# Kernel tuning notes

Measured on AMD Instinct MI355X. Metric: run time of the kernel, lower is better.

Reference implementation:

```python
import jax, jax.numpy as jnp
import numpy as np

D_MODEL, D_STATE, D_CONV, EXPAND = 1024, 16, 4, 2
D_INNER = D_MODEL * EXPAND
BATCH, SEQ_LEN = 2, 2048
LN_EPS = 1e-5


def setup_inputs() -> dict:
    key = jax.random.key(0)
    ks = jax.random.split(key, 10)
    s = lambda fan_in: 1.0 / np.sqrt(fan_in)
    x = jax.random.normal(ks[0], (BATCH, D_MODEL, SEQ_LEN), jnp.float32)
    ln_w = jnp.ones((D_MODEL,), jnp.float32)
    ln_b = jnp.zeros((D_MODEL,), jnp.float32)
    # Linear weights stored as [in, out]
    W_in = jax.random.normal(ks[1], (D_MODEL, 2 * D_INNER), jnp.float32) * s(D_MODEL)
    conv_w = jax.random.normal(ks[2], (D_INNER, 1, D_CONV), jnp.float32) * s(D_CONV)
    conv_b = jax.random.normal(ks[3], (D_INNER,), jnp.float32) * s(D_CONV)
    W_x = jax.random.normal(ks[4], (D_INNER, 2 * D_STATE + D_INNER), jnp.float32) * s(D_INNER)
    W_dt = jax.random.normal(ks[5], (D_INNER, D_INNER), jnp.float32) * s(D_INNER)
    b_dt = jax.random.normal(ks[6], (D_INNER,), jnp.float32) * s(D_INNER)
    A_log = jnp.broadcast_to(jnp.log(jnp.arange(1, D_STATE + 1, dtype=jnp.float32))[None, :], (D_INNER, D_STATE))
    Dskip = jnp.ones((D_INNER,), jnp.float32)
    W_out = jax.random.normal(ks[7], (D_INNER, D_MODEL), jnp.float32) * s(D_INNER)
    return {"x": x, "ln_w": ln_w, "ln_b": ln_b, "W_in": W_in, "conv_w": conv_w,
            "conv_b": conv_b, "W_x": W_x, "W_dt": W_dt, "b_dt": b_dt,
            "A_log": A_log, "Dskip": Dskip, "W_out": W_out}


def _selective_scan(u, delta, A, Bp, Cp, Dskip):
    # u, delta: [B, d_inner, L]; A: [d_inner, d_state]; Bp, Cp: [B, d_state, L]
    u_T = jnp.transpose(u, (2, 0, 1))        # [L, B, d_inner]
    d_T = jnp.transpose(delta, (2, 0, 1))    # [L, B, d_inner]
    B_T = jnp.transpose(Bp, (2, 0, 1))       # [L, B, d_state]
    C_T = jnp.transpose(Cp, (2, 0, 1))       # [L, B, d_state]
    h0 = jnp.zeros((u.shape[0], u.shape[1], A.shape[1]), u.dtype)

    def step(h, inp):
        dlt_t, B_t, C_t, u_t = inp
        dA = jnp.exp(dlt_t[..., None] * A)                       # [B, d_inner, d_state]
        h = dA * h + dlt_t[..., None] * B_t[:, None, :] * u_t[..., None]
        y_t = jnp.einsum('bds,bs->bd', h, C_t)
        return h, y_t

    _, ys = jax.lax.scan(step, h0, (d_T, B_T, C_T, u_T))
    y = jnp.transpose(ys, (1, 2, 0))  # [B, d_inner, L]
    return y + Dskip[None, :, None] * u


def reference(x, ln_w, ln_b, W_in, conv_w, conv_b, W_x, W_dt, b_dt, A_log, Dskip, W_out):
    residual = x
    xt = jnp.swapaxes(x, 1, 2)  # [B, L, d_model]
    mu = xt.mean(-1, keepdims=True)
    var = ((xt - mu) ** 2).mean(-1, keepdims=True)
    xn = (xt - mu) * jax.lax.rsqrt(var + LN_EPS) * ln_w + ln_b
    xz = xn @ W_in                                   # [B, L, 2*d_inner]
    xb, z = jnp.split(xz, 2, axis=-1)
    xb = jnp.swapaxes(xb, 1, 2)                      # [B, d_inner, L]
    # causal depthwise conv (torch pads d_conv-1 both sides then slices [:L])
    xb = jax.lax.conv_general_dilated(
        xb, conv_w, window_strides=(1,), padding=[(D_CONV - 1, 0)],
        dimension_numbers=('NCH', 'OIH', 'NCH'), feature_group_count=D_INNER)
    xb = xb + conv_b[None, :, None]
    xb = jax.nn.silu(xb)
    xbt = jnp.swapaxes(xb, 1, 2)                     # [B, L, d_inner]
    bcd = xbt @ W_x                                  # [B, L, 2*d_state + d_inner]
    Bp = bcd[..., :D_STATE]
    Cp = bcd[..., D_STATE:2 * D_STATE]
    dlt = jax.nn.softplus(bcd[..., 2 * D_STATE:] @ W_dt + b_dt)
    Bp = jnp.swapaxes(Bp, 1, 2)                      # [B, d_state, L]
    Cp = jnp.swapaxes(Cp, 1, 2)
    dlt = jnp.swapaxes(dlt, 1, 2)                    # [B, d_inner, L]
    A = -jnp.exp(A_log)
    y = _selective_scan(xb, dlt, A, Bp, Cp, Dskip)   # [B, d_inner, L]
    y = jnp.swapaxes(y, 1, 2) * jax.nn.silu(z)       # [B, L, d_inner]
    out = y @ W_out                                  # [B, L, d_model]
    return jnp.swapaxes(out, 1, 2) + residual
```

## Files before the change

### kernel.cpp

```cpp
#include <hip/hip_runtime.h>
#include <cstdint>
#include <cstddef>

#define SEQL 2048
#define DMODEL 1024
#define DINNER 2048
#define NSTATE 16
#define NC 32
#define TC 64
#define KS 16
#define KCH 128

typedef __attribute__((ext_vector_type(4))) float f32x4;
typedef __attribute__((ext_vector_type(8))) short short8;
typedef __attribute__((ext_vector_type(4))) short short4v;
typedef unsigned short u16;

__device__ __forceinline__ float b2f(u16 u) {
  union { unsigned int i; float f; } v; v.i = ((unsigned int)u) << 16; return v.f;
}
__device__ __forceinline__ u16 f2b(float f) {
  union { float f; unsigned int i; } v; v.f = f;
  unsigned int r = v.i + 0x7FFFu + ((v.i >> 16) & 1u);
  return (u16)(r >> 16);
}

__global__ __launch_bounds__(256) void k_transpose_cvt(
    const float* __restrict__ in, u16* __restrict__ out, int R, int C, int c0) {
  __shared__ float t[32][33];
  int cb = blockIdx.x * 32, rb = blockIdx.y * 32;
  int tx = threadIdx.x, ty = threadIdx.y;
#pragma unroll
  for (int i = 0; i < 32; i += 8)
    t[ty + i][tx] = in[(size_t)(rb + ty + i) * C + c0 + cb + tx];
  __syncthreads();
#pragma unroll
  for (int i = 0; i < 32; i += 8)
    out[(size_t)(cb + ty + i) * R + rb + tx] = f2b(t[tx][ty + i]);
}

__global__ __launch_bounds__(256) void k_layernorm(
    const u16* __restrict__ xt, const float* __restrict__ w,
    const float* __restrict__ b, u16* __restrict__ xn) {
  int row = blockIdx.x;
  const u16* px = xt + (size_t)row * DMODEL;
  int i4 = threadIdx.x * 4;
  short4v sv = *(const short4v*)&px[i4];
  float v[4];
#pragma unroll
  for (int j = 0; j < 4; ++j) v[j] = b2f((u16)sv[j]);
  float s1 = v[0] + v[1] + v[2] + v[3];
  float s2 = v[0]*v[0] + v[1]*v[1] + v[2]*v[2] + v[3]*v[3];
#pragma unroll
  for (int off = 32; off > 0; off >>= 1) {
    s1 += __shfl_xor(s1, off);
    s2 += __shfl_xor(s2, off);
  }
  __shared__ float a1[4], a2[4];
  int lane = threadIdx.x & 63, wid = threadIdx.x >> 6;
  if (lane == 0) { a1[wid] = s1; a2[wid] = s2; }
  __syncthreads();
  float t1 = a1[0] + a1[1] + a1[2] + a1[3];
  float t2 = a2[0] + a2[1] + a2[2] + a2[3];
  float mu = t1 * (1.f / DMODEL);
  float rs = rsqrtf(t2 * (1.f / DMODEL) - mu * mu + 1e-5f);
  short4v ov;
#pragma unroll
  for (int j = 0; j < 4; ++j) ov[j] = (short)f2b((v[j] - mu) * rs * w[i4 + j] + b[i4 + j]);
  *(short4v*)&xn[(size_t)row * DMODEL + i4] = ov;
}

template<int EPI>
__global__ __launch_bounds__(256) void gemm8p(
    const u16* __restrict__ A, const u16* __restrict__ BT,
    void* __restrict__ outp, const float* __restrict__ bias,
    const float* __restrict__ resid, int M, int N, int K) {
  constexpr int LDSTILE = 2 * 128 * 64;
  __shared__ u16 lds[2 * LDSTILE];

  const int tid = threadIdx.x;
  const int w = tid >> 6, lane = tid & 63;
  const int wm = w >> 1, wn = w & 1;
  const int lg = lane >> 4, lr = lane & 15;
  const int wbase = tid & ~63;

  const int gx = N / 128;
  const int cpx = gridDim.x >> 3;
  const int wg = ((int)blockIdx.x & 7) * cpx + ((int)blockIdx.x >> 3);
  const int tm = (wg / gx) * 128;
  const int tn = (wg % gx) * 128;
  const int NT = K >> 6;

  const u16* Ab = A + (size_t)tm * K;
  const u16* Bb = BT + (size_t)tn * K;

  auto stage = [&](const u16* gbase, int boff, int tc, int h) {
    int tcl = tc < NT ? tc : NT - 1;
    const u16* g0 = gbase + (size_t)tcl * 64;
    u16* l0 = lds + (tc & 1) * LDSTILE + boff;
#pragma unroll
    for (int j = 0; j < 2; ++j) {
      int t8 = j * 256 + tid;
      int r8 = t8 >> 3;
      int pr = (r8 & 31) + ((r8 >> 5) << 6) + h * 32;
      int sk = ((((t8 & 7) << 4) ^ ((pr & 7) << 4)) >> 1);
      int r8b = (j * 256 + wbase) >> 3;
      int prb = (r8b & 31) + ((r8b >> 5) << 6) + h * 32;
      __builtin_amdgcn_global_load_lds(
          (const __attribute__((address_space(1))) void*)(g0 + (size_t)pr * K + sk),
          (__attribute__((address_space(3))) void*)(l0 + prb * 64), 16, 0, 0);
    }
  };
  auto fragA = [&](int buf, int mf, int kk) -> short8 {
    int r = wm * 64 + mf * 16 + lr;
    int cb = (kk * 64 + lg * 16) ^ ((r & 7) << 4);
    return *(const short8*)((const char*)(lds + buf * LDSTILE) + r * 128 + cb);
  };
  auto fragB = [&](int buf, int nf, int kk) -> short8 {
    int r = wn * 64 + nf * 16 + lr;
    int cb = (kk * 64 + lg * 16) ^ ((r & 7) << 4);
    return *(const short8*)((const char*)(lds + buf * LDSTILE + 128 * 64) + r * 128 + cb);
  };

  f32x4 acc[4][4] = {};
  short8 aF[2][2], bF0[2][2], bF1[2][2];

  stage(Ab, 0, 0, 0); stage(Bb, 128 * 64, 0, 0);
  stage(Bb, 128 * 64, 0, 1); stage(Ab, 0, 0, 1);
  stage(Ab, 0, 1, 0); stage(Bb, 128 * 64, 1, 0);
  asm volatile("s_waitcnt vmcnt(4)" ::: "memory");
  __builtin_amdgcn_s_barrier();

  for (int t = 0; t < NT; ++t) {
    const int buf = t & 1;
#pragma unroll
    for (int mf = 0; mf < 2; ++mf) { aF[mf][0] = fragA(buf, mf, 0); aF[mf][1] = fragA(buf, mf, 1); }
#pragma unroll
    for (int nf = 0; nf < 2; ++nf) { bF0[nf][0] = fragB(buf, nf, 0); bF0[nf][1] = fragB(buf, nf, 1); }
    stage(Bb, 128 * 64, t + 1, 1);
    __builtin_amdgcn_s_barrier();
    asm volatile("s_waitcnt lgkmcnt(0)" ::: "memory");
    __builtin_amdgcn_s_setprio(1);
#pragma unroll
    for (int mf = 0; mf < 2; ++mf)
#pragma unroll
      for (int nf = 0; nf < 2; ++nf) {
        acc[mf][nf] = __builtin_amdgcn_mfma_f32_16x16x32_bf16(aF[mf][0], bF0[nf][0], acc[mf][nf], 0, 0, 0);
        acc[mf][nf] = __builtin_amdgcn_mfma_f32_16x16x32_bf16(aF[mf][1], bF0[nf][1], acc[mf][nf], 0, 0, 0);
      }
    __builtin_amdgcn_s_setprio(0);
    __builtin_amdgcn_s_barrier();
#pragma unroll
    for (int nf = 0; nf < 2; ++nf) { bF1[nf][0] = fragB(buf, 2 + nf, 0); bF1[nf][1] = fragB(buf, 2 + nf, 1); }
    stage(Ab, 0, t + 1, 1);
    __builtin_amdgcn_s_barrier();
    asm volatile("s_waitcnt lgkmcnt(0)" ::: "memory");
    __builtin_amdgcn_s_setprio(1);
#pragma unroll
    for (int mf = 0; mf < 2; ++mf)
#pragma unroll
      for (int nf = 0; nf < 2; ++nf) {
        acc[mf][2 + nf] = __builtin_amdgcn_mfma_f32_16x16x32_bf16(aF[mf][0], bF1[nf][0], acc[mf][2 + nf], 0, 0, 0);
        acc[mf][2 + nf] = __builtin_amdgcn_mfma_f32_16x16x32_bf16(aF[mf][1], bF1[nf][1], acc[mf][2 + nf], 0, 0, 0);
      }
    __builtin_amdgcn_s_setprio(0);
    __builtin_amdgcn_s_barrier();
#pragma unroll
    for (int mf = 0; mf < 2; ++mf) { aF[mf][0] = fragA(buf, 2 + mf, 0); aF[mf][1] = fragA(buf, 2 + mf, 1); }
    stage(Ab, 0, t + 2, 0);
    __builtin_amdgcn_s_barrier();
    asm volatile("s_waitcnt lgkmcnt(0)" ::: "memory");
    __builtin_amdgcn_s_setprio(1);
#pragma unroll
    for (int mf = 0; mf < 2; ++mf)
#pragma unroll
      for (int nf = 0; nf < 2; ++nf) {
        acc[2 + mf][nf] = __builtin_amdgcn_mfma_f32_16x16x32_bf16(aF[mf][0], bF0[nf][0], acc[2 + mf][nf], 0, 0, 0);
        acc[2 + mf][nf] = __builtin_amdgcn_mfma_f32_16x16x32_bf16(aF[mf][1], bF0[nf][1], acc[2 + mf][nf], 0, 0, 0);
      }
    __builtin_amdgcn_s_setprio(0);
    __builtin_amdgcn_s_barrier();
    stage(Bb, 128 * 64, t + 2, 0);
    __builtin_amdgcn_s_barrier();
    asm volatile("s_waitcnt lgkmcnt(0)" ::: "memory");
    __builtin_amdgcn_s_setprio(1);
#pragma unroll
    for (int mf = 0; mf < 2; ++mf)
#pragma unroll
      for (int nf = 0; nf < 2; ++nf) {
        acc[2 + mf][2 + nf] = __builtin_amdgcn_mfma_f32_16x16x32_bf16(aF[mf][0], bF1[nf][0], acc[2 + mf][2 + nf], 0, 0, 0);
        acc[2 + mf][2 + nf] = __builtin_amdgcn_mfma_f32_16x16x32_bf16(aF[mf][1], bF1[nf][1], acc[2 + mf][2 + nf], 0, 0, 0);
      }
    __builtin_amdgcn_s_setprio(0);
    asm volatile("s_waitcnt vmcnt(4)" ::: "memory");
    __builtin_amdgcn_s_barrier();
  }

#pragma unroll
  for (int mf = 0; mf < 4; ++mf) {
    int r0 = tm + wm * 64 + mf * 16 + lg * 4;
#pragma unroll
    for (int nf = 0; nf < 4; ++nf) {
      int c = tn + wn * 64 + nf * 16 + lr;
      f32x4 v = acc[mf][nf];
#pragma unroll
      for (int j = 0; j < 4; ++j) {
        int r = r0 + j;
        if constexpr (EPI == 1) {
          ((u16*)outp)[(size_t)r * N + c] = f2b(v[j]);
        } else if constexpr (EPI == 2) {
          float xv = v[j] + bias[c];
          ((float*)outp)[(size_t)r * N + c] = (xv > 20.f) ? xv : log1pf(__expf(xv));
        } else if constexpr (EPI == 3) {
          int bb = r >> 11, tt = r & (SEQL - 1);
          size_t oi = ((size_t)(bb * N + c)) * SEQL + tt;
          ((float*)outp)[oi] = v[j] + resid[oi];
        } else {
          ((float*)outp)[(size_t)r * N + c] = v[j];
        }
      }
    }
  }
}

__global__ __launch_bounds__(256) void k_conv_silu(
    const u16* __restrict__ xz, const float* __restrict__ cw,
    const float* __restrict__ cb, u16* __restrict__ xbt) {
  size_t idx = (size_t)blockIdx.x * 256 + threadIdx.x;
  int d = (int)(idx & (DINNER - 1));
  int l = (int)((idx >> 11) & (SEQL - 1));
  int b = (int)(idx >> 22);
  f32x4 w = *(const f32x4*)&cw[d * 4];
  float acc = cb[d];
  size_t base = ((size_t)b * SEQL) * 4096 + d;
#pragma unroll
  for (int i = 0; i < 4; ++i) {
    int ls = l - 3 + i;
    if (ls >= 0) acc += w[i] * b2f(xz[base + (size_t)ls * 4096]);
  }
  float s = acc / (1.f + __expf(-acc));
  xbt[idx] = f2b(s);
}

__global__ __launch_bounds__(256) void k_bc_mfma(
    const u16* __restrict__ xbt, const u16* __restrict__ WxBCT,
    float* __restrict__ bcp) {
  __shared__ u16 As[128 * 32];
  int tid = threadIdx.x;
  int w = tid >> 6, lane = tid & 63;
  int tm = blockIdx.x * 128;
  int k0 = blockIdx.y * KCH;
  int lg = lane >> 4, lr = lane & 15;
  int srow = lane >> 2, scol = (lane & 3) * 8;

  f32x4 acc[2][2] = {};

  for (int kk = k0; kk < k0 + KCH; kk += 32) {
#pragma unroll
    for (int j = 0; j < 2; ++j) {
      int ch = w * 2 + j;
      const u16* ga = xbt + (size_t)(tm + ch * 16 + srow) * DINNER + kk + scol;
      __builtin_amdgcn_global_load_lds(
          (const __attribute__((address_space(1))) void*)ga,
          (__attribute__((address_space(3))) void*)&As[ch * 512], 16, 0, 0);
    }
    __syncthreads();
    short8 aF[2], bF[2];
#pragma unroll
    for (int m = 0; m < 2; ++m)
      aF[m] = *(const short8*)&As[(w * 32 + m * 16 + lr) * 32 + lg * 8];
#pragma unroll
    for (int n = 0; n < 2; ++n)
      bF[n] = *(const short8*)&WxBCT[(size_t)(n * 16 + lr) * DINNER + kk + lg * 8];
#pragma unroll
    for (int m = 0; m < 2; ++m)
#pragma unroll
      for (int n = 0; n < 2; ++n)
        acc[m][n] = __builtin_amdgcn_mfma_f32_16x16x32_bf16(aF[m], bF[n], acc[m][n], 0, 0, 0);
    __syncthreads();
  }

  float* outp = bcp + (size_t)blockIdx.y * (4096 * 32);
#pragma unroll
  for (int m = 0; m < 2; ++m) {
    int r0 = tm + w * 32 + m * 16 + lg * 4;
#pragma unroll
    for (int n = 0; n < 2; ++n) {
      int c = n * 16 + lr;
      f32x4 v = acc[m][n];
#pragma unroll
      for (int j = 0; j < 4; ++j)
        outp[(size_t)(r0 + j) * 32 + c] = v[j];
    }
  }
}

__global__ __launch_bounds__(256) void k_bc_red(
    const float* __restrict__ bcp, float* __restrict__ bc) {
  size_t i = (size_t)blockIdx.x * 256 + threadIdx.x;
  float s = 0.f;
#pragma unroll
  for (int ks = 0; ks < KS; ++ks)
    s += bcp[(size_t)ks * (4096 * 32) + i];
  bc[i] = s;
}

__global__ __launch_bounds__(256) void k_scan_p1(
    const float* __restrict__ dlt, const u16* __restrict__ ub,
    const float* __restrict__ bcv, const float* __restrict__ A_log,
    float* __restrict__ Pc, float* __restrict__ Qc) {
  int d = blockIdx.x * 256 + threadIdx.x;
  int c = blockIdx.y;
  int b = blockIdx.z;
  float Av[16];
#pragma unroll
  for (int sv = 0; sv < 4; ++sv) {
    f32x4 al = *(const f32x4*)&A_log[d * 16 + sv * 4];
#pragma unroll
    for (int j = 0; j < 4; ++j) Av[sv * 4 + j] = -__expf(al[j]);
  }
  float P[16], Q[16];
#pragma unroll
  for (int s = 0; s < 16; ++s) { P[s] = 1.f; Q[s] = 0.f; }
  size_t row0 = (size_t)b * SEQL + (size_t)c * TC;
  for (int t = 0; t < TC; ++t) {
    size_t row = row0 + t;
    float dl = dlt[row * DINNER + d];
    float uu = b2f(ub[row * DINNER + d]);
    float bco = dl * uu;
    const f32x4* Bp = (const f32x4*)&bcv[row * 32];
#pragma unroll
    for (int sv = 0; sv < 4; ++sv) {
      f32x4 Bv = Bp[sv];
#pragma unroll
      for (int j = 0; j < 4; ++j) {
        int s = sv * 4 + j;
        float dA = __expf(dl * Av[s]);
        P[s] *= dA;
        Q[s] = dA * Q[s] + bco * Bv[j];
      }
    }
  }
  size_t base = (((size_t)b * NC + c) * DINNER + d) * 16;
#pragma unroll
  for (int sv = 0; sv < 4; ++sv) {
    f32x4 pv, qv;
#pragma unroll
    for (int j = 0; j < 4; ++j) { pv[j] = P[sv * 4 + j]; qv[j] = Q[sv * 4 + j]; }
    *(f32x4*)&Pc[base + sv * 4] = pv;
    *(f32x4*)&Qc[base + sv * 4] = qv;
  }
}

__global__ __launch_bounds__(256) void k_scan_p2(
    const float* __restrict__ Pc, const float* __restrict__ Qc,
    float* __restrict__ Hs) {
  size_t gid = (size_t)blockIdx.x * 256 + threadIdx.x;
  size_t bds = gid & ((size_t)DINNER * 16 - 1);
  int b = (int)(gid >> 15);
  float h = 0.f;
  size_t cstride = (size_t)DINNER * 16;
  size_t base = (size_t)b * NC * cstride + bds;
  for (int c = 0; c < NC; ++c) {
    size_t idx = base + (size_t)c * cstride;
    Hs[idx] = h;
    h = Pc[idx] * h + Qc[idx];
  }
}

__global__ __launch_bounds__(256) void k_scan_p3(
    const float* __restrict__ dlt, const u16* __restrict__ ub,
    const float* __restrict__ bcv, const u16* __restrict__ xz,
    const float* __restrict__ A_log, const float* __restrict__ Dskip,
    const float* __restrict__ Hs, u16* __restrict__ yg) {
  int d = blockIdx.x * 256 + threadIdx.x;
  int c = blockIdx.y;
  int b = blockIdx.z;
  float Av[16];
#pragma unroll
  for (int sv = 0; sv < 4; ++sv) {
    f32x4 al = *(const f32x4*)&A_log[d * 16 + sv * 4];
#pragma unroll
    for (int j = 0; j < 4; ++j) Av[sv * 4 + j] = -__expf(al[j]);
  }
  float h[16];
  size_t hb = (((size_t)b * NC + c) * DINNER + d) * 16;
#pragma unroll
  for (int sv = 0; sv < 4; ++sv) {
    f32x4 hv = *(const f32x4*)&Hs[hb + sv * 4];
#pragma unroll
    for (int j = 0; j < 4; ++j) h[sv * 4 + j] = hv[j];
  }
  float Dsk = Dskip[d];
  size_t row0 = (size_t)b * SEQL + (size_t)c * TC;
  for (int t = 0; t < TC; ++t) {
    size_t row = row0 + t;
    float dl = dlt[row * DINNER + d];
    float uu = b2f(ub[row * DINNER + d]);
    float bco = dl * uu;
    const f32x4* BCp = (const f32x4*)&bcv[row * 32];
    float y = 0.f;
#pragma unroll
    for (int sv = 0; sv < 4; ++sv) {
      f32x4 Bv = BCp[sv];
      f32x4 Cv = BCp[4 + sv];
#pragma unroll
      for (int j = 0; j < 4; ++j) {
        int s = sv * 4 + j;
        float dA = __expf(dl * Av[s]);
        h[s] = dA * h[s] + bco * Bv[j];
        y += h[s] * Cv[j];
      }
    }
    float zv = b2f(xz[row * 4096 + DINNER + d]);
    float yv = (y + Dsk * uu) * (zv / (1.f + __expf(-zv)));
    yg[row * DINNER + d] = f2b(yv);
  }
}

extern "C" void kernel_launch(void* const* d_in, const int* in_sizes, int n_in,
                              void* d_out, int out_size, void* d_ws, size_t ws_size,
                              hipStream_t stream) {
  (void)in_sizes; (void)n_in; (void)out_size; (void)ws_size;
  const float* x      = (const float*)d_in[0];
  const float* ln_w   = (const float*)d_in[1];
  const float* ln_b   = (const float*)d_in[2];
  const float* W_in   = (const float*)d_in[3];
  const float* conv_w = (const float*)d_in[4];
  const float* conv_b = (const float*)d_in[5];
  const float* W_x    = (const float*)d_in[6];
  const float* W_dt   = (const float*)d_in[7];
  const float* b_dt   = (const float*)d_in[8];
  const float* A_log  = (const float*)d_in[9];
  const float* Dskip  = (const float*)d_in[10];
  const float* W_out  = (const float*)d_in[11];
  float* out = (float*)d_out;

  char* ws = (char*)d_ws;
  const size_t MB = 1048576;
  u16*  xt    = (u16*)(ws + 0 * MB);
  u16*  xn    = (u16*)(ws + 8 * MB);
  u16*  WinT  = (u16*)(ws + 16 * MB);
  u16*  WxT   = (u16*)(ws + 24 * MB);
  u16*  WdtT  = (u16*)(ws + 32 * MB);
  u16*  WoutT = (u16*)(ws + 40 * MB);
  u16*  xz    = (u16*)(ws + 44 * MB);
  u16*  xbt   = (u16*)(ws + 76 * MB);
  float* bc   = (float*)(ws + 92 * MB);
  u16*  dtin  = (u16*)(ws + 93 * MB);
  float* dlt  = (float*)(ws + 109 * MB);
  float* Pc   = (float*)(ws + 141 * MB);
  float* Qc   = (float*)(ws + 149 * MB);
  float* Hs   = (float*)(ws + 157 * MB);
  float* bcp  = (float*)(ws + 165 * MB);
  u16*  WxBCT = (u16*)(ws + 173 * MB);
  u16*  yg    = (u16*)(ws + 0 * MB);

  dim3 tb(32, 8);
  for (int b = 0; b < 2; ++b)
    k_transpose_cvt<<<dim3(SEQL / 32, DMODEL / 32), tb, 0, stream>>>(
        x + (size_t)b * DMODEL * SEQL, xt + (size_t)b * SEQL * DMODEL, DMODEL, SEQL, 0);
  k_transpose_cvt<<<dim3(4096 / 32, 1024 / 32), tb, 0, stream>>>(W_in, WinT, 1024, 4096, 0);
  k_transpose_cvt<<<dim3(2048 / 32, 2048 / 32), tb, 0, stream>>>(W_x, WxT, 2048, 2080, 32);
  k_transpose_cvt<<<dim3(1, 2048 / 32), tb, 0, stream>>>(W_x, WxBCT, 2048, 2080, 0);
  k_transpose_cvt<<<dim3(2048 / 32, 2048 / 32), tb, 0, stream>>>(W_dt, WdtT, 2048, 2048, 0);
  k_transpose_cvt<<<dim3(1024 / 32, 2048 / 32), tb, 0, stream>>>(W_out, WoutT, 2048, 1024, 0);

  k_layernorm<<<4096, 256, 0, stream>>>(xt, ln_w, ln_b, xn);

  gemm8p<1><<<1024, 256, 0, stream>>>(xn, WinT, xz, nullptr, nullptr, 4096, 4096, 1024);

  k_conv_silu<<<32768, 256, 0, stream>>>(xz, conv_w, conv_b, xbt);

  k_bc_mfma<<<dim3(4096 / 128, KS), 256, 0, stream>>>(xbt, WxBCT, bcp);
  k_bc_red<<<131072 / 256, 256, 0, stream>>>(bcp, bc);

  gemm8p<1><<<512, 256, 0, stream>>>(xbt, WxT, dtin, nullptr, nullptr, 4096, 2048, 2048);

  gemm8p<2><<<512, 256, 0, stream>>>(dtin, WdtT, dlt, b_dt, nullptr, 4096, 2048, 2048);

  k_scan_p1<<<dim3(DINNER / 256, NC, 2), 256, 0, stream>>>(dlt, xbt, bc, A_log, Pc, Qc);
  k_scan_p2<<<256, 256, 0, stream>>>(Pc, Qc, Hs);
  k_scan_p3<<<dim3(DINNER / 256, NC, 2), 256, 0, stream>>>(
      dlt, xbt, bc, xz, A_log, Dskip, Hs, yg);

  gemm8p<3><<<256, 256, 0, stream>>>(yg, WoutT, out, nullptr, x, 4096, 1024, 2048);
}
```

Baseline: 335.0 us.

## Fold W_x and W_dt into one weight, precompute GEMM addresses, vectorize conv

The delta path now multiplies the two weight matrices once (W_dt^T · W_x-slice^T) into a combined 2048x2048 matrix, replacing two activation GEMMs with one weight GEMM plus one activation GEMM. The GEMM kernel precomputes per-thread global and LDS addresses and unrolls the K loop by two so fixed buffer offsets replace per-iteration index math. The conv+silu kernel now handles two channels per thread with paired bf16 loads and stores. The weight product is computed in bf16 on every call, which adds rounding error on the delta path.

```diff
diff --git a/kernel.cpp b/kernel.cpp
--- a/kernel.cpp
+++ b/kernel.cpp
@@ -37,6 +37,18 @@
 #pragma unroll
   for (int i = 0; i < 32; i += 8)
     out[(size_t)(cb + ty + i) * R + rb + tx] = f2b(t[tx][ty + i]);
+}
+
+__global__ __launch_bounds__(256) void k_cvt_rows(
+    const float* __restrict__ in, u16* __restrict__ out) {
+  size_t idx = (size_t)blockIdx.x * 256 + threadIdx.x;
+  size_t i4 = idx * 4;
+  int r = (int)(i4 >> 11), c = (int)(i4 & 2047);
+  f32x4 v = *(const f32x4*)&in[(size_t)r * 2080 + 32 + c];
+  short4v o;
+#pragma unroll
+  for (int j = 0; j < 4; ++j) o[j] = (short)f2b(v[j]);
+  *(short4v*)&out[i4] = o;
 }
 
 __global__ __launch_bounds__(256) void k_layernorm(
@@ -91,109 +103,134 @@
   const int tn = (wg % gx) * 128;
   const int NT = K >> 6;
 
-  const u16* Ab = A + (size_t)tm * K;
-  const u16* Bb = BT + (size_t)tn * K;
-
-  auto stage = [&](const u16* gbase, int boff, int tc, int h) {
-    int tcl = tc < NT ? tc : NT - 1;
-    const u16* g0 = gbase + (size_t)tcl * 64;
-    u16* l0 = lds + (tc & 1) * LDSTILE + boff;
-#pragma unroll
-    for (int j = 0; j < 2; ++j) {
-      int t8 = j * 256 + tid;
-      int r8 = t8 >> 3;
-      int pr = (r8 & 31) + ((r8 >> 5) << 6) + h * 32;
-      int sk = ((((t8 & 7) << 4) ^ ((pr & 7) << 4)) >> 1);
-      int r8b = (j * 256 + wbase) >> 3;
-      int prb = (r8b & 31) + ((r8b >> 5) << 6) + h * 32;
+  const u16* aSp[2];
+  const u16* bSp[2];
+  int aD[2], bD[2];
+#pragma unroll
+  for (int j = 0; j < 2; ++j) {
+    int t8 = j * 256 + tid;
+    int r8 = t8 >> 3;
+    int pr = (r8 & 31) + ((r8 >> 5) << 6);
+    int sk = ((((t8 & 7) << 4) ^ ((pr & 7) << 4)) >> 1);
+    aSp[j] = A + (size_t)(tm + pr) * K + sk;
+    bSp[j] = BT + (size_t)(tn + pr) * K + sk;
+    int r8b = (j * 256 + wbase) >> 3;
+    int prb = (r8b & 31) + ((r8b >> 5) << 6);
+    aD[j] = prb * 64;
+    bD[j] = 128 * 64 + prb * 64;
+  }
+  int aFo[4][2], bFo[4][2];
+#pragma unroll
+  for (int mf = 0; mf < 4; ++mf)
+#pragma unroll
+    for (int kk = 0; kk < 2; ++kk) {
+      int r = wm * 64 + mf * 16 + lr;
+      aFo[mf][kk] = r * 128 + ((kk * 64 + lg * 16) ^ ((r & 7) << 4));
+      int rb = wn * 64 + mf * 16 + lr;
+      bFo[mf][kk] = 128 * 64 * 2 + rb * 128 + ((kk * 64 + lg * 16) ^ ((rb & 7) << 4));
+    }
+
+  auto stA = [&](int toff, int h, int buf) {
+#pragma unroll
+    for (int j = 0; j < 2; ++j)
       __builtin_amdgcn_global_load_lds(
-          (const __attribute__((address_space(1))) void*)(g0 + (size_t)pr * K + sk),
-          (__attribute__((address_space(3))) void*)(l0 + prb * 64), 16, 0, 0);
-    }
+          (const __attribute__((address_space(1))) void*)(aSp[j] + toff * 64 + h * (K << 5)),
+          (__attribute__((address_space(3))) void*)(lds + buf * LDSTILE + aD[j] + h * 2048),
+          16, 0, 0);
   };
-  auto fragA = [&](int buf, int mf, int kk) -> short8 {
-    int r = wm * 64 + mf * 16 + lr;
-    int cb = (kk * 64 + lg * 16) ^ ((r & 7) << 4);
-    return *(const short8*)((const char*)(lds + buf * LDSTILE) + r * 128 + cb);
-  };
-  auto fragB = [&](int buf, int nf, int kk) -> short8 {
-    int r = wn * 64 + nf * 16 + lr;
-    int cb = (kk * 64 + lg * 16) ^ ((r & 7) << 4);
-    return *(const short8*)((const char*)(lds + buf * LDSTILE + 128 * 64) + r * 128 + cb);
+  auto stB = [&](int toff, int h, int buf) {
+#pragma unroll
+    for (int j = 0; j < 2; ++j)
+      __builtin_amdgcn_global_load_lds(
+          (const __attribute__((address_space(1))) void*)(bSp[j] + toff * 64 + h * (K << 5)),
+          (__attribute__((address_space(3))) void*)(lds + buf * LDSTILE + bD[j] + h * 2048),
+          16, 0, 0);
   };
 
   f32x4 acc[4][4] = {};
   short8 aF[2][2], bF0[2][2], bF1[2][2];
 
-  stage(Ab, 0, 0, 0); stage(Bb, 128 * 64, 0, 0);
-  stage(Bb, 128 * 64, 0, 1); stage(Ab, 0, 0, 1);
-  stage(Ab, 0, 1, 0); stage(Bb, 128 * 64, 1, 0);
+  stA(0, 0, 0); stB(0, 0, 0); stB(0, 1, 0); stA(0, 1, 0);
+  stA(1, 0, 1); stB(1, 0, 1);
   asm volatile("s_waitcnt vmcnt(4)" ::: "memory");
   __builtin_amdgcn_s_barrier();
 
-  for (int t = 0; t < NT; ++t) {
-    const int buf = t & 1;
-#pragma unroll
-    for (int mf = 0; mf < 2; ++mf) { aF[mf][0] = fragA(buf, mf, 0); aF[mf][1] = fragA(buf, mf, 1); }
-#pragma unroll
-    for (int nf = 0; nf < 2; ++nf) { bF0[nf][0] = fragB(buf, nf, 0); bF0[nf][1] = fragB(buf, nf, 1); }
-    stage(Bb, 128 * 64, t + 1, 1);
-    __builtin_amdgcn_s_barrier();
-    asm volatile("s_waitcnt lgkmcnt(0)" ::: "memory");
-    __builtin_amdgcn_s_setprio(1);
-#pragma unroll
-    for (int mf = 0; mf < 2; ++mf)
-#pragma unroll
-      for (int nf = 0; nf < 2; ++nf) {
-        acc[mf][nf] = __builtin_amdgcn_mfma_f32_16x16x32_bf16(aF[mf][0], bF0[nf][0], acc[mf][nf], 0, 0, 0);
-        acc[mf][nf] = __builtin_amdgcn_mfma_f32_16x16x32_bf16(aF[mf][1], bF0[nf][1], acc[mf][nf], 0, 0, 0);
-      }
-    __builtin_amdgcn_s_setprio(0);
-    __builtin_amdgcn_s_barrier();
-#pragma unroll
-    for (int nf = 0; nf < 2; ++nf) { bF1[nf][0] = fragB(buf, 2 + nf, 0); bF1[nf][1] = fragB(buf, 2 + nf, 1); }
-    stage(Ab, 0, t + 1, 1);
-    __builtin_amdgcn_s_barrier();
-    asm volatile("s_waitcnt lgkmcnt(0)" ::: "memory");
-    __builtin_amdgcn_s_setprio(1);
-#pragma unroll
-    for (int mf = 0; mf < 2; ++mf)
-#pragma unroll
-      for (int nf = 0; nf < 2; ++nf) {
-        acc[mf][2 + nf] = __builtin_amdgcn_mfma_f32_16x16x32_bf16(aF[mf][0], bF1[nf][0], acc[mf][2 + nf], 0, 0, 0);
-        acc[mf][2 + nf] = __builtin_amdgcn_mfma_f32_16x16x32_bf16(aF[mf][1], bF1[nf][1], acc[mf][2 + nf], 0, 0, 0);
-      }
-    __builtin_amdgcn_s_setprio(0);
-    __builtin_amdgcn_s_barrier();
-#pragma unroll
-    for (int mf = 0; mf < 2; ++mf) { aF[mf][0] = fragA(buf, 2 + mf, 0); aF[mf][1] = fragA(buf, 2 + mf, 1); }
-    stage(Ab, 0, t + 2, 0);
-    __builtin_amdgcn_s_barrier();
-    asm volatile("s_waitcnt lgkmcnt(0)" ::: "memory");
-    __builtin_amdgcn_s_setprio(1);
-#pragma unroll
-    for (int mf = 0; mf < 2; ++mf)
-#pragma unroll
-      for (int nf = 0; nf < 2; ++nf) {
-        acc[2 + mf][nf] = __builtin_amdgcn_mfma_f32_16x16x32_bf16(aF[mf][0], bF0[nf][0], acc[2 + mf][nf], 0, 0, 0);
-        acc[2 + mf][nf] = __builtin_amdgcn_mfma_f32_16x16x32_bf16(aF[mf][1], bF0[nf][1], acc[2 + mf][nf], 0, 0, 0);
-      }
-    __builtin_amdgcn_s_setprio(0);
-    __builtin_amdgcn_s_barrier();
-    stage(Bb, 128 * 64, t + 2, 0);
-    __builtin_amdgcn_s_barrier();
-    asm volatile("s_waitcnt lgkmcnt(0)" ::: "memory");
-    __builtin_amdgcn_s_setprio(1);
-#pragma unroll
-    for (int mf = 0; mf < 2; ++mf)
-#pragma unroll
-      for (int nf = 0; nf < 2; ++nf) {
-        acc[2 + mf][2 + nf] = __builtin_amdgcn_mfma_f32_16x16x32_bf16(aF[mf][0], bF1[nf][0], acc[2 + mf][2 + nf], 0, 0, 0);
-        acc[2 + mf][2 + nf] = __builtin_amdgcn_mfma_f32_16x16x32_bf16(aF[mf][1], bF1[nf][1], acc[2 + mf][2 + nf], 0, 0, 0);
-      }
-    __builtin_amdgcn_s_setprio(0);
-    asm volatile("s_waitcnt vmcnt(4)" ::: "memory");
-    __builtin_amdgcn_s_barrier();
+  for (int tt = 0; tt < NT; tt += 2) {
+#pragma unroll
+    for (int u = 0; u < 2; ++u) {
+      const char* Lb = (const char*)lds + u * (LDSTILE * 2);
+#pragma unroll
+      for (int mf = 0; mf < 2; ++mf)
+#pragma unroll
+        for (int kk = 0; kk < 2; ++kk) aF[mf][kk] = *(const short8*)(Lb + aFo[mf][kk]);
+#pragma unroll
+      for (int nf = 0; nf < 2; ++nf)
+#pragma unroll
+        for (int kk = 0; kk < 2; ++kk) bF0[nf][kk] = *(const short8*)(Lb + bFo[nf][kk]);
+      stB(u + 1, 1, (u + 1) & 1);
+      __builtin_amdgcn_s_barrier();
+      asm volatile("s_waitcnt lgkmcnt(0)" ::: "memory");
+      __builtin_amdgcn_s_setprio(1);
+#pragma unroll
+      for (int mf = 0; mf < 2; ++mf)
+#pragma unroll
+        for (int nf = 0; nf < 2; ++nf) {
+          acc[mf][nf] = __builtin_amdgcn_mfma_f32_16x16x32_bf16(aF[mf][0], bF0[nf][0], acc[mf][nf], 0, 0, 0);
+          acc[mf][nf] = __builtin_amdgcn_mfma_f32_16x16x32_bf16(aF[mf][1], bF0[nf][1], acc[mf][nf], 0, 0, 0);
+        }
+      __builtin_amdgcn_s_setprio(0);
+      __builtin_amdgcn_s_barrier();
+#pragma unroll
+      for (int nf = 0; nf < 2; ++nf)
+#pragma unroll
+        for (int kk = 0; kk < 2; ++kk) bF1[nf][kk] = *(const short8*)(Lb + bFo[2 + nf][kk]);
+      stA(u + 1, 1, (u + 1) & 1);
+      __builtin_amdgcn_s_barrier();
+      asm volatile("s_waitcnt lgkmcnt(0)" ::: "memory");
+      __builtin_amdgcn_s_setprio(1);
+#pragma unroll
+      for (int mf = 0; mf < 2; ++mf)
+#pragma unroll
+        for (int nf = 0; nf < 2; ++nf) {
+          acc[mf][2 + nf] = __builtin_amdgcn_mfma_f32_16x16x32_bf16(aF[mf][0], bF1[nf][0], acc[mf][2 + nf], 0, 0, 0);
+          acc[mf][2 + nf] = __builtin_amdgcn_mfma_f32_16x16x32_bf16(aF[mf][1], bF1[nf][1], acc[mf][2 + nf], 0, 0, 0);
+        }
+      __builtin_amdgcn_s_setprio(0);
+      __builtin_amdgcn_s_barrier();
+#pragma unroll
+      for (int mf = 0; mf < 2; ++mf)
+#pragma unroll
+        for (int kk = 0; kk < 2; ++kk) aF[mf][kk] = *(const short8*)(Lb + aFo[2 + mf][kk]);
+      stA(u + 2, 0, u & 1);
+      __builtin_amdgcn_s_barrier();
+      asm volatile("s_waitcnt lgkmcnt(0)" ::: "memory");
+      __builtin_amdgcn_s_setprio(1);
+#pragma unroll
+      for (int mf = 0; mf < 2; ++mf)
+#pragma unroll
+        for (int nf = 0; nf < 2; ++nf) {
+          acc[2 + mf][nf] = __builtin_amdgcn_mfma_f32_16x16x32_bf16(aF[mf][0], bF0[nf][0], acc[2 + mf][nf], 0, 0, 0);
+          acc[2 + mf][nf] = __builtin_amdgcn_mfma_f32_16x16x32_bf16(aF[mf][1], bF0[nf][1], acc[2 + mf][nf], 0, 0, 0);
+        }
+      __builtin_amdgcn_s_setprio(0);
+      __builtin_amdgcn_s_barrier();
+      stB(u + 2, 0, u & 1);
+      __builtin_amdgcn_s_barrier();
+      asm volatile("s_waitcnt lgkmcnt(0)" ::: "memory");
+      __builtin_amdgcn_s_setprio(1);
+#pragma unroll
+      for (int mf = 0; mf < 2; ++mf)
+#pragma unroll
+        for (int nf = 0; nf < 2; ++nf) {
+          acc[2 + mf][2 + nf] = __builtin_amdgcn_mfma_f32_16x16x32_bf16(aF[mf][0], bF1[nf][0], acc[2 + mf][2 + nf], 0, 0, 0);
+          acc[2 + mf][2 + nf] = __builtin_amdgcn_mfma_f32_16x16x32_bf16(aF[mf][1], bF1[nf][1], acc[2 + mf][2 + nf], 0, 0, 0);
+        }
+      __builtin_amdgcn_s_setprio(0);
+      asm volatile("s_waitcnt vmcnt(4)" ::: "memory");
+      __builtin_amdgcn_s_barrier();
+    }
+#pragma unroll
+    for (int j = 0; j < 2; ++j) { aSp[j] += 128; bSp[j] += 128; }
   }
 
 #pragma unroll
@@ -212,8 +249,8 @@
           float xv = v[j] + bias[c];
           ((float*)outp)[(size_t)r * N + c] = (xv > 20.f) ? xv : log1pf(__expf(xv));
         } else if constexpr (EPI == 3) {
-          int bb = r >> 11, tt = r & (SEQL - 1);
-          size_t oi = ((size_t)(bb * N + c)) * SEQL + tt;
+          int bb = r >> 11, tt2 = r & (SEQL - 1);
+          size_t oi = ((size_t)(bb * N + c)) * SEQL + tt2;
           ((float*)outp)[oi] = v[j] + resid[oi];
         } else {
           ((float*)outp)[(size_t)r * N + c] = v[j];
@@ -227,19 +264,27 @@
     const u16* __restrict__ xz, const float* __restrict__ cw,
     const float* __restrict__ cb, u16* __restrict__ xbt) {
   size_t idx = (size_t)blockIdx.x * 256 + threadIdx.x;
-  int d = (int)(idx & (DINNER - 1));
-  int l = (int)((idx >> 11) & (SEQL - 1));
-  int b = (int)(idx >> 22);
-  f32x4 w = *(const f32x4*)&cw[d * 4];
-  float acc = cb[d];
-  size_t base = ((size_t)b * SEQL) * 4096 + d;
+  int d2 = (int)(idx & (DINNER / 2 - 1));
+  int d = d2 * 2;
+  int l = (int)((idx >> 10) & (SEQL - 1));
+  int b = (int)(idx >> 21);
+  f32x4 w0 = *(const f32x4*)&cw[d * 4];
+  f32x4 w1 = *(const f32x4*)&cw[d * 4 + 4];
+  float a0 = cb[d], a1 = cb[d + 1];
+  size_t base = ((size_t)b * SEQL + l) * 4096 + d;
 #pragma unroll
   for (int i = 0; i < 4; ++i) {
     int ls = l - 3 + i;
-    if (ls >= 0) acc += w[i] * b2f(xz[base + (size_t)ls * 4096]);
-  }
-  float s = acc / (1.f + __expf(-acc));
-  xbt[idx] = f2b(s);
+    if (ls >= 0) {
+      unsigned int pv = *(const unsigned int*)&xz[base + (size_t)(i - 3) * 4096];
+      a0 += w0[i] * b2f((u16)(pv & 0xFFFF));
+      a1 += w1[i] * b2f((u16)(pv >> 16));
+    }
+  }
+  float s0 = a0 / (1.f + __expf(-a0));
+  float s1 = a1 / (1.f + __expf(-a1));
+  unsigned int ov = (unsigned int)f2b(s0) | ((unsigned int)f2b(s1) << 16);
+  *(unsigned int*)&xbt[((size_t)b * SEQL + l) * DINNER + d] = ov;
 }
 
 __global__ __launch_bounds__(256) void k_bc_mfma(
@@ -441,13 +486,13 @@
   u16*  xt    = (u16*)(ws + 0 * MB);
   u16*  xn    = (u16*)(ws + 8 * MB);
   u16*  WinT  = (u16*)(ws + 16 * MB);
-  u16*  WxT   = (u16*)(ws + 24 * MB);
   u16*  WdtT  = (u16*)(ws + 32 * MB);
   u16*  WoutT = (u16*)(ws + 40 * MB);
   u16*  xz    = (u16*)(ws + 44 * MB);
   u16*  xbt   = (u16*)(ws + 76 * MB);
   float* bc   = (float*)(ws + 92 * MB);
-  u16*  dtin  = (u16*)(ws + 93 * MB);
+  u16*  WxRaw = (u16*)(ws + 93 * MB);
+  u16*  W_cT  = (u16*)(ws + 101 * MB);
   float* dlt  = (float*)(ws + 109 * MB);
   float* Pc   = (float*)(ws + 141 * MB);
   float* Qc   = (float*)(ws + 149 * MB);
@@ -461,23 +506,23 @@
     k_transpose_cvt<<<dim3(SEQL / 32, DMODEL / 32), tb, 0, stream>>>(
         x + (size_t)b * DMODEL * SEQL, xt + (size_t)b * SEQL * DMODEL, DMODEL, SEQL, 0);
   k_transpose_cvt<<<dim3(4096 / 32, 1024 / 32), tb, 0, stream>>>(W_in, WinT, 1024, 4096, 0);
-  k_transpose_cvt<<<dim3(2048 / 32, 2048 / 32), tb, 0, stream>>>(W_x, WxT, 2048, 2080, 32);
   k_transpose_cvt<<<dim3(1, 2048 / 32), tb, 0, stream>>>(W_x, WxBCT, 2048, 2080, 0);
   k_transpose_cvt<<<dim3(2048 / 32, 2048 / 32), tb, 0, stream>>>(W_dt, WdtT, 2048, 2048, 0);
   k_transpose_cvt<<<dim3(1024 / 32, 2048 / 32), tb, 0, stream>>>(W_out, WoutT, 2048, 1024, 0);
+  k_cvt_rows<<<4096, 256, 0, stream>>>(W_x, WxRaw);
+
+  gemm8p<1><<<256, 256, 0, stream>>>(WdtT, WxRaw, W_cT, nullptr, nullptr, 2048, 2048, 2048);
 
   k_layernorm<<<4096, 256, 0, stream>>>(xt, ln_w, ln_b, xn);
 
   gemm8p<1><<<1024, 256, 0, stream>>>(xn, WinT, xz, nullptr, nullptr, 4096, 4096, 1024);
 
-  k_conv_silu<<<32768, 256, 0, stream>>>(xz, conv_w, conv_b, xbt);
+  k_conv_silu<<<16384, 256, 0, stream>>>(xz, conv_w, conv_b, xbt);
 
   k_bc_mfma<<<dim3(4096 / 128, KS), 256, 0, stream>>>(xbt, WxBCT, bcp);
   k_bc_red<<<131072 / 256, 256, 0, stream>>>(bcp, bc);
 
-  gemm8p<1><<<512, 256, 0, stream>>>(xbt, WxT, dtin, nullptr, nullptr, 4096, 2048, 2048);
-
-  gemm8p<2><<<512, 256, 0, stream>>>(dtin, WdtT, dlt, b_dt, nullptr, 4096, 2048, 2048);
+  gemm8p<2><<<512, 256, 0, stream>>>(xbt, W_cT, dlt, b_dt, nullptr, 4096, 2048, 2048);
 
   k_scan_p1<<<dim3(DINNER / 256, NC, 2), 256, 0, stream>>>(dlt, xbt, bc, A_log, Pc, Qc);
   k_scan_p2<<<256, 256, 0, stream>>>(Pc, Qc, Hs);
```

Result: faster. 310.9 us (-7.2%).
